# Kernel optimization log

Measured on AMD Instinct MI355X. Metric: run time of the kernel, lower is better.

The kernel has to match this reference:

```python
import jax, jax.numpy as jnp
import numpy as np

B, N, C = 4, 2048, 1024
H = 8
D = C // H  # head dim = 128
SCALE = D ** -0.5
EPS = 1e-5


def setup_inputs() -> dict:
    key = jax.random.key(0)
    ks = jax.random.split(key, 12)
    s = 0.02
    return {
        "x": jax.random.normal(ks[0], (B, N, C), jnp.float32),
        "ln1_g": jnp.ones((C,), jnp.float32),
        "ln1_b": jnp.zeros((C,), jnp.float32),
        "w_qkv": jax.random.normal(ks[1], (3 * C, C), jnp.float32) * s,  # torch Linear weight [out,in], no bias
        "w_proj": jax.random.normal(ks[2], (C, C), jnp.float32) * s,
        "b_proj": jnp.zeros((C,), jnp.float32),
        "ln2_g": jnp.ones((C,), jnp.float32),
        "ln2_b": jnp.zeros((C,), jnp.float32),
        "w1": jax.random.normal(ks[3], (C, C), jnp.float32) * s,
        "b1": jnp.full((C,), 0.1, jnp.float32),
        "w2": jax.random.normal(ks[4], (C, C), jnp.float32) * s,
        "b2": jnp.full((C,), 0.1, jnp.float32),
        "bn_g": jnp.ones((C,), jnp.float32),
        "bn_b": jnp.zeros((C,), jnp.float32),
        "bn_mean": jnp.zeros((C,), jnp.float32),
        "bn_var": jnp.ones((C,), jnp.float32),
    }


def _layernorm(x, g, b):
    mu = jnp.mean(x, axis=-1, keepdims=True)
    var = jnp.mean(jnp.square(x - mu), axis=-1, keepdims=True)
    return (x - mu) * jax.lax.rsqrt(var + EPS) * g + b


def reference(x, ln1_g, ln1_b, w_qkv, w_proj, b_proj, ln2_g, ln2_b,
              w1, b1, w2, b2, bn_g, bn_b, bn_mean, bn_var):
    # --- attention branch (pre-LN) ---
    h = _layernorm(x, ln1_g, ln1_b)
    qkv = h @ w_qkv.T                              # [B,N,3C]
    qkv = qkv.reshape(B, N, 3, H, D)
    q = qkv[:, :, 0].transpose(0, 2, 1, 3)         # [B,H,N,D]
    k = qkv[:, :, 1].transpose(0, 2, 1, 3)
    v = qkv[:, :, 2].transpose(0, 2, 1, 3)
    attn = jnp.einsum('bhnd,bhmd->bhnm', q, k) * SCALE
    attn = jax.nn.softmax(attn, axis=-1)
    o = jnp.einsum('bhnm,bhmd->bhnd', attn, v)     # [B,H,N,D]
    o = o.transpose(0, 2, 1, 3).reshape(B, N, C)
    x = x + (o @ w_proj.T + b_proj)

    # --- MLP branch (pre-LN), ELU + eval-mode BatchNorm ---
    h = _layernorm(x, ln2_g, ln2_b)
    h = jax.nn.elu(h @ w1.T + b1)
    h = jax.nn.elu(h @ w2.T + b2)
    h = (h - bn_mean) * jax.lax.rsqrt(bn_var + EPS) * bn_g + bn_b
    return x + h
```

## Files before the change

kernel.cpp:

```cpp
#include <hip/hip_runtime.h>
#include <hip/hip_bf16.h>

using u16 = unsigned short;
typedef __attribute__((ext_vector_type(8))) __bf16 bf16x8;
typedef __attribute__((ext_vector_type(4))) float f32x4;
typedef __attribute__((ext_vector_type(16))) float f32x16;
typedef __attribute__((ext_vector_type(4))) unsigned int u32x4;

#define LN_EPS 1e-5f
#define ATT_SCALE 0.08838834764831845f

__device__ __forceinline__ u16 f2bf(float f) {
    unsigned int u = __builtin_bit_cast(unsigned int, f);
    u += 0x7FFFu + ((u >> 16) & 1u);
    return (u16)(u >> 16);
}

__device__ __forceinline__ bf16x8 ld_frag(const u16* p) {
    return __builtin_bit_cast(bf16x8, *(const u32x4*)p);
}

__device__ __forceinline__ unsigned pack_bf2(float lo, float hi) {
    return __builtin_amdgcn_perm(__builtin_bit_cast(unsigned, hi),
                                 __builtin_bit_cast(unsigned, lo), 0x07060302u);
}

__device__ __forceinline__ void gl_lds(const u16* g, u16* l) {
    __builtin_amdgcn_global_load_lds((const __attribute__((address_space(1))) void*)g,
                                     (__attribute__((address_space(3))) void*)l, 16, 0, 0);
}

__global__ void cvt_all(const float* __restrict__ w_qkv, const float* __restrict__ w_proj,
                        const float* __restrict__ w1, const float* __restrict__ w2,
                        u16* __restrict__ out) {
    const int i = blockIdx.x * blockDim.x + threadIdx.x;
    const int n_qkv = 3072 * 1024 / 4, n_c = 1024 * 1024 / 4;
    const float* src;
    int j = i;
    if (j < n_qkv) { src = w_qkv; }
    else if ((j -= n_qkv) < n_c) { src = w_proj; }
    else if ((j -= n_c) < n_c)   { src = w1; }
    else { j -= n_c; src = w2; }
    const float4 v = ((const float4*)src)[j];
    ushort4 o;
    o.x = f2bf(v.x); o.y = f2bf(v.y); o.z = f2bf(v.z); o.w = f2bf(v.w);
    ((ushort4*)out)[i] = o;
}

__global__ __launch_bounds__(256)
void ln_kernel(const float* __restrict__ x, const float* __restrict__ g,
               const float* __restrict__ b, u16* __restrict__ out)
{
    const int row = blockIdx.x;
    const int t = threadIdx.x;
    const float4 v = ((const float4*)(x + (size_t)row * 1024))[t];
    float s  = v.x + v.y + v.z + v.w;
    float ss = v.x * v.x + v.y * v.y + v.z * v.z + v.w * v.w;
    #pragma unroll
    for (int d = 32; d > 0; d >>= 1) { s += __shfl_down(s, d); ss += __shfl_down(ss, d); }
    __shared__ float red[8];
    const int wave = t >> 6, lane = t & 63;
    if (lane == 0) { red[wave] = s; red[4 + wave] = ss; }
    __syncthreads();
    const float S  = red[0] + red[1] + red[2] + red[3];
    const float SS = red[4] + red[5] + red[6] + red[7];
    const float mu = S * (1.f / 1024.f);
    const float rstd = rsqrtf(SS * (1.f / 1024.f) - mu * mu + LN_EPS);
    const float4 gv = ((const float4*)g)[t];
    const float4 bv = ((const float4*)b)[t];
    ushort4 ov;
    ov.x = f2bf((v.x - mu) * rstd * gv.x + bv.x);
    ov.y = f2bf((v.y - mu) * rstd * gv.y + bv.y);
    ov.z = f2bf((v.z - mu) * rstd * gv.z + bv.z);
    ov.w = f2bf((v.w - mu) * rstd * gv.w + bv.w);
    ((ushort4*)(out + (size_t)row * 1024))[t] = ov;
}

__global__ __launch_bounds__(256, 3)
void gemm_qkv(const u16* __restrict__ A, const u16* __restrict__ Bw,
              u16* __restrict__ Cb, u16* __restrict__ Cv)
{
    const int K = 1024;
    __shared__ __align__(16) u16 As[128 * 32];
    __shared__ __align__(16) u16 Bs[128 * 32];

    const int tid  = threadIdx.x;
    const int wave = tid >> 6;
    const int lane = tid & 63;
    const int quad = lane >> 4;
    const int l16  = lane & 15;
    const int m0 = blockIdx.x * 128;
    const int n0 = blockIdx.y * 128;
    const int wm = (wave & 1) * 64;
    const int wn = (wave >> 1) * 64;

    f32x4 acc[4][4];
    #pragma unroll
    for (int i = 0; i < 4; i++)
        #pragma unroll
        for (int j = 0; j < 4; j++)
            acc[i][j] = f32x4{0.f, 0.f, 0.f, 0.f};

    const int srow = lane >> 2;
    const int scol = (lane & 3) * 8;
    const u16* gA0 = A  + (size_t)(m0 + wave * 32 + srow) * K + scol;
    const u16* gA1 = gA0 + (size_t)16 * K;
    const u16* gB0 = Bw + (size_t)(n0 + wave * 32 + srow) * K + scol;
    const u16* gB1 = gB0 + (size_t)16 * K;
    u16* lA0 = &As[(wave * 32) * 32];
    u16* lA1 = &As[(wave * 32 + 16) * 32];
    u16* lB0 = &Bs[(wave * 32) * 32];
    u16* lB1 = &Bs[(wave * 32 + 16) * 32];

    for (int k0 = 0; k0 < K; k0 += 32) {
        gl_lds(gA0 + k0, lA0);
        gl_lds(gA1 + k0, lA1);
        gl_lds(gB0 + k0, lB0);
        gl_lds(gB1 + k0, lB1);
        __syncthreads();
        bf16x8 af[4], bfv[4];
        #pragma unroll
        for (int i = 0; i < 4; i++) af[i]  = ld_frag(&As[(wm + i * 16 + l16) * 32 + quad * 8]);
        #pragma unroll
        for (int j = 0; j < 4; j++) bfv[j] = ld_frag(&Bs[(wn + j * 16 + l16) * 32 + quad * 8]);
        #pragma unroll
        for (int i = 0; i < 4; i++)
            #pragma unroll
            for (int j = 0; j < 4; j++)
                acc[i][j] = __builtin_amdgcn_mfma_f32_16x16x32_bf16(af[i], bfv[j], acc[i][j], 0, 0, 0);
        __syncthreads();
    }

    #pragma unroll
    for (int j = 0; j < 4; j++) {
        const int gn = n0 + wn + j * 16 + l16;
        if (gn < 2048) {
            const float qs = (gn < 1024) ? ATT_SCALE : 1.0f;
            #pragma unroll
            for (int i = 0; i < 4; i++) {
                const int gm0 = m0 + wm + i * 16 + quad * 4;
                #pragma unroll
                for (int r = 0; r < 4; r++)
                    Cb[(size_t)(gm0 + r) * 2048 + gn] = f2bf(acc[i][j][r] * qs);
            }
        } else {
            const int hh = (gn >> 7) & 7, dd = gn & 127;
            #pragma unroll
            for (int i = 0; i < 4; i++) {
                const int gm0 = m0 + wm + i * 16 + quad * 4;
                #pragma unroll
                for (int r = 0; r < 4; r++) {
                    const int tok = gm0 + r;
                    Cv[((size_t)((tok >> 11) * 8 + hh) * 128 + dd) * 2048 + (tok & 2047)] =
                        f2bf(acc[i][j][r]);
                }
            }
        }
    }
}

template <int EPI>
__global__ __launch_bounds__(256, 3)
void gemm_c(const u16* __restrict__ A, const u16* __restrict__ Bw,
            const float* __restrict__ bias, const float* __restrict__ res,
            float* __restrict__ Cf, u16* __restrict__ Cb,
            const float* __restrict__ bng, const float* __restrict__ bnb,
            const float* __restrict__ bnm, const float* __restrict__ bnv)
{
    const int N = 1024, K = 1024;
    __shared__ __align__(16) u16 As[128 * 32];
    __shared__ __align__(16) u16 Bs[128 * 32];

    const int tid  = threadIdx.x;
    const int wave = tid >> 6;
    const int lane = tid & 63;
    const int quad = lane >> 4;
    const int l16  = lane & 15;
    const int m0 = blockIdx.x * 128;
    const int n0 = blockIdx.y * 128;
    const int wm = (wave & 1) * 64;
    const int wn = (wave >> 1) * 64;

    f32x4 acc[4][4];
    #pragma unroll
    for (int i = 0; i < 4; i++)
        #pragma unroll
        for (int j = 0; j < 4; j++)
            acc[i][j] = f32x4{0.f, 0.f, 0.f, 0.f};

    const int srow = lane >> 2;
    const int scol = (lane & 3) * 8;
    const u16* gA0 = A  + (size_t)(m0 + wave * 32 + srow) * K + scol;
    const u16* gA1 = gA0 + (size_t)16 * K;
    const u16* gB0 = Bw + (size_t)(n0 + wave * 32 + srow) * K + scol;
    const u16* gB1 = gB0 + (size_t)16 * K;
    u16* lA0 = &As[(wave * 32) * 32];
    u16* lA1 = &As[(wave * 32 + 16) * 32];
    u16* lB0 = &Bs[(wave * 32) * 32];
    u16* lB1 = &Bs[(wave * 32 + 16) * 32];

    for (int k0 = 0; k0 < K; k0 += 32) {
        gl_lds(gA0 + k0, lA0);
        gl_lds(gA1 + k0, lA1);
        gl_lds(gB0 + k0, lB0);
        gl_lds(gB1 + k0, lB1);
        __syncthreads();
        bf16x8 af[4], bfv[4];
        #pragma unroll
        for (int i = 0; i < 4; i++) af[i]  = ld_frag(&As[(wm + i * 16 + l16) * 32 + quad * 8]);
        #pragma unroll
        for (int j = 0; j < 4; j++) bfv[j] = ld_frag(&Bs[(wn + j * 16 + l16) * 32 + quad * 8]);
        #pragma unroll
        for (int i = 0; i < 4; i++)
            #pragma unroll
            for (int j = 0; j < 4; j++)
                acc[i][j] = __builtin_amdgcn_mfma_f32_16x16x32_bf16(af[i], bfv[j], acc[i][j], 0, 0, 0);
        __syncthreads();
    }

    #pragma unroll
    for (int j = 0; j < 4; j++) {
        const int gn = n0 + wn + j * 16 + l16;
        float bs = bias[gn], sc = 0.f, sh = 0.f;
        if constexpr (EPI == 3) {
            const float iv = rsqrtf(bnv[gn] + LN_EPS);
            sc = bng[gn] * iv;
            sh = bnb[gn] - bnm[gn] * sc;
        }
        #pragma unroll
        for (int i = 0; i < 4; i++) {
            const int gm0 = m0 + wm + i * 16 + quad * 4;
            #pragma unroll
            for (int r = 0; r < 4; r++) {
                const size_t idx = (size_t)(gm0 + r) * N + gn;
                const float v = acc[i][j][r];
                if constexpr (EPI == 1) {
                    Cf[idx] = res[idx] + v + bs;
                } else if constexpr (EPI == 2) {
                    float t = v + bs;
                    t = t > 0.f ? t : (__expf(t) - 1.f);
                    Cb[idx] = f2bf(t);
                } else {
                    float t = v + bs;
                    t = t > 0.f ? t : (__expf(t) - 1.f);
                    t = t * sc + sh;
                    Cf[idx] = res[idx] + t;
                }
            }
        }
    }
}

__global__ __launch_bounds__(256, 2)
void attn_kernel(const u16* __restrict__ qk, const u16* __restrict__ vT, u16* __restrict__ o)
{
    __shared__ __align__(16) u16 smem[32768];

    const int tid  = threadIdx.x;
    const int wave = tid >> 6;
    const int lane = tid & 63;
    const int l32  = lane & 31;
    const int hl   = lane >> 5;
    const int id   = blockIdx.x;
    const int bh   = ((id >> 7) << 3) | (id & 7);
    const int qt   = (id >> 3) & 15;
    const int b    = bh >> 3, h = bh & 7;
    const size_t tok0 = (size_t)b * 2048;

    const u16* qptr = qk + h * 128;
    const u16* kptr = qk + 1024 + h * 128;
    const u16* vptr = vT + (size_t)bh * 128 * 2048;

    #pragma unroll
    for (int qq = 0; qq < 8; qq++) {
        const int s = qq * 256 + tid;
        const int r = s >> 4;
        const int cg = (s & 15) ^ (r & 7);
        const u16* g = qptr + (tok0 + qt * 128 + r) * 2048 + cg * 8;
        const int sb = 16384 + (qq * 256 + (tid & 192)) * 8;
        gl_lds(g, smem + sb);
    }
    __syncthreads();

    bf16x8 qf[8];
    {
        const int row = wave * 32 + l32;
        #pragma unroll
        for (int ks = 0; ks < 8; ks++) {
            const int c = (ks * 2 + hl) ^ (row & 7);
            qf[ks] = ld_frag(smem + 16384 + row * 128 + c * 8);
        }
    }

    f32x16 oacc[4];
    #pragma unroll
    for (int i = 0; i < 4; i++)
        #pragma unroll
        for (int e = 0; e < 16; e++) oacc[i][e] = 0.f;
    float l_acc = 0.f;

    {
        #pragma unroll
        for (int qq = 0; qq < 4; qq++) {
            const int s = qq * 256 + tid;
            const int rk = s >> 4, ck = (s & 15) ^ (rk & 7);
            gl_lds(kptr + (tok0 + rk) * 2048 + ck * 8,
                   smem + (qq * 256 + (tid & 192)) * 8);
            const int rv = s >> 3, cv = (s & 7) ^ (rv & 7);
            gl_lds(vptr + (size_t)rv * 2048 + cv * 8,
                   smem + 8192 + (qq * 256 + (tid & 192)) * 8);
        }
    }

    for (int kt = 0; kt < 32; kt++) {
        __syncthreads();

        if (kt + 1 < 32) {
            u16* nb = smem + ((kt + 1) & 1) * 16384;
            #pragma unroll
            for (int qq = 0; qq < 4; qq++) {
                const int s = qq * 256 + tid;
                const int rk = s >> 4, ck = (s & 15) ^ (rk & 7);
                gl_lds(kptr + (tok0 + (kt + 1) * 64 + rk) * 2048 + ck * 8,
                       nb + (qq * 256 + (tid & 192)) * 8);
                const int rv = s >> 3, cv = (s & 7) ^ (rv & 7);
                gl_lds(vptr + (size_t)rv * 2048 + (kt + 1) * 64 + cv * 8,
                       nb + 8192 + (qq * 256 + (tid & 192)) * 8);
            }
        }

        const u16* Ks = smem + (kt & 1) * 16384;
        const u16* Vs = Ks + 8192;

        f32x16 sacc[2];
        #pragma unroll
        for (int t = 0; t < 2; t++)
            #pragma unroll
            for (int e = 0; e < 16; e++) sacc[t][e] = 0.f;
        #pragma unroll
        for (int ks = 0; ks < 8; ks++) {
            #pragma unroll
            for (int mt = 0; mt < 2; mt++) {
                const int row = mt * 32 + l32;
                const int c = (ks * 2 + hl) ^ (row & 7);
                const bf16x8 kf = ld_frag(Ks + row * 128 + c * 8);
                sacc[mt] = __builtin_amdgcn_mfma_f32_32x32x16_bf16(kf, qf[ks], sacc[mt], 0, 0, 0);
            }
        }

        unsigned pk[2][8];
        #pragma unroll
        for (int t = 0; t < 2; t++) {
            #pragma unroll
            for (int r2 = 0; r2 < 8; r2++) {
                const float p0 = __expf(sacc[t][2 * r2]);
                const float p1 = __expf(sacc[t][2 * r2 + 1]);
                l_acc += p0 + p1;
                pk[t][r2] = pack_bf2(p0, p1);
            }
        }

        #pragma unroll
        for (int ks = 0; ks < 4; ks++) {
            const int t = ks >> 1;
            const int pb = (ks & 1) * 4;
            const unsigned s0 = (unsigned)__shfl_xor((int)pk[t][pb + 0], 32);
            const unsigned s1 = (unsigned)__shfl_xor((int)pk[t][pb + 1], 32);
            const unsigned s2 = (unsigned)__shfl_xor((int)pk[t][pb + 2], 32);
            const unsigned s3 = (unsigned)__shfl_xor((int)pk[t][pb + 3], 32);
            u32x4 pu;
            pu.x = hl ? s2 : pk[t][pb + 0];
            pu.y = hl ? s3 : pk[t][pb + 1];
            pu.z = hl ? pk[t][pb + 2] : s0;
            pu.w = hl ? pk[t][pb + 3] : s1;
            const bf16x8 pf = __builtin_bit_cast(bf16x8, pu);
            #pragma unroll
            for (int dt = 0; dt < 4; dt++) {
                const int row = dt * 32 + l32;
                const int c = (ks * 2 + hl) ^ (row & 7);
                const bf16x8 vf = ld_frag(Vs + row * 64 + c * 8);
                oacc[dt] = __builtin_amdgcn_mfma_f32_32x32x16_bf16(vf, pf, oacc[dt], 0, 0, 0);
            }
        }
    }

    __syncthreads();
    u16* Ot = smem;
    const float lt  = l_acc + __shfl_xor(l_acc, 32);
    const float inv = 1.0f / lt;
    const int qloc = wave * 32 + l32;
    #pragma unroll
    for (int dt = 0; dt < 4; dt++) {
        #pragma unroll
        for (int r2 = 0; r2 < 8; r2++) {
            const float v0 = oacc[dt][2 * r2] * inv;
            const float v1 = oacc[dt][2 * r2 + 1] * inv;
            const int dp = dt * 32 + 4 * hl + 2 * (r2 & 1) + 8 * (r2 >> 1);
            *(unsigned*)(Ot + qloc * 136 + dp) = pack_bf2(v0, v1);
        }
    }
    __syncthreads();
    const int qr = tid >> 1;
    const int hh = tid & 1;
    const u16* src = Ot + qr * 136 + hh * 64;
    u16* dst = o + (tok0 + qt * 128 + qr) * 1024 + h * 128 + hh * 64;
    #pragma unroll
    for (int c = 0; c < 8; c++)
        *(u32x4*)(dst + c * 8) = *(const u32x4*)(src + c * 8);
}

extern "C" void kernel_launch(void* const* d_in, const int* in_sizes, int n_in,
                              void* d_out, int out_size, void* d_ws, size_t ws_size,
                              hipStream_t stream)
{
    const float* x      = (const float*)d_in[0];
    const float* ln1_g  = (const float*)d_in[1];
    const float* ln1_b  = (const float*)d_in[2];
    const float* w_qkv  = (const float*)d_in[3];
    const float* w_proj = (const float*)d_in[4];
    const float* b_proj = (const float*)d_in[5];
    const float* ln2_g  = (const float*)d_in[6];
    const float* ln2_b  = (const float*)d_in[7];
    const float* w1     = (const float*)d_in[8];
    const float* b1     = (const float*)d_in[9];
    const float* w2     = (const float*)d_in[10];
    const float* b2     = (const float*)d_in[11];
    const float* bn_g   = (const float*)d_in[12];
    const float* bn_b   = (const float*)d_in[13];
    const float* bn_m   = (const float*)d_in[14];
    const float* bn_v   = (const float*)d_in[15];
    float* out = (float*)d_out;

    u16* wq   = (u16*)d_ws;
    u16* wp   = wq  + (size_t)3072 * 1024;
    u16* w1b  = wp  + (size_t)1024 * 1024;
    u16* w2b  = w1b + (size_t)1024 * 1024;
    u16* hbuf = w2b + (size_t)1024 * 1024;
    u16* qkb  = hbuf + (size_t)8192 * 1024;
    u16* vTb  = qkb + (size_t)8192 * 2048;
    u16* obuf = vTb + (size_t)8192 * 1024;
    float* x1 = (float*)(obuf + (size_t)8192 * 1024);

    cvt_all<<<6144, 256, 0, stream>>>(w_qkv, w_proj, w1, w2, wq);

    ln_kernel<<<8192, 256, 0, stream>>>(x, ln1_g, ln1_b, hbuf);

    gemm_qkv<<<dim3(64, 24), 256, 0, stream>>>(hbuf, wq, qkb, vTb);

    attn_kernel<<<512, 256, 0, stream>>>(qkb, vTb, obuf);

    gemm_c<1><<<dim3(64, 8), 256, 0, stream>>>(obuf, wp,
        b_proj, x, x1, nullptr, nullptr, nullptr, nullptr, nullptr);

    ln_kernel<<<8192, 256, 0, stream>>>(x1, ln2_g, ln2_b, hbuf);

    gemm_c<2><<<dim3(64, 8), 256, 0, stream>>>(hbuf, w1b,
        b1, nullptr, nullptr, obuf, nullptr, nullptr, nullptr, nullptr);

    gemm_c<3><<<dim3(64, 8), 256, 0, stream>>>(obuf, w2b,
        b2, x1, out, nullptr, bn_g, bn_b, bn_m, bn_v);
}
```

Measured before the change: 394.7 us.

## Split attention key tiles across two wave groups with LDS reduction

The attention block grows from 256 to 512 threads. Each of the two wave groups handles half of every 64-key tile, so each wave does one S MFMA chain instead of two. The partial O accumulators and row sums are then combined through LDS in two phases before normalisation and the bf16 store. It also swaps the shfl_xor lane exchange for permlane32_swap where that builtin exists. This is meant to raise occupancy and latency hiding, at the cost of extra barriers, a cross-group reduction, and a changed V swizzle.

```diff
diff --git a/kernel.cpp b/kernel.cpp
--- a/kernel.cpp
+++ b/kernel.cpp
@@ -6,6 +6,7 @@
 typedef __attribute__((ext_vector_type(4))) float f32x4;
 typedef __attribute__((ext_vector_type(16))) float f32x16;
 typedef __attribute__((ext_vector_type(4))) unsigned int u32x4;
+typedef __attribute__((ext_vector_type(2))) unsigned int uint2v;
 
 #define LN_EPS 1e-5f
 #define ATT_SCALE 0.08838834764831845f
@@ -251,13 +252,15 @@
     }
 }
 
-__global__ __launch_bounds__(256, 2)
+__global__ __launch_bounds__(512, 4)
 void attn_kernel(const u16* __restrict__ qk, const u16* __restrict__ vT, u16* __restrict__ o)
 {
     __shared__ __align__(16) u16 smem[32768];
 
     const int tid  = threadIdx.x;
     const int wave = tid >> 6;
+    const int g    = wave & 3;
+    const int kh   = wave >> 2;
     const int lane = tid & 63;
     const int l32  = lane & 31;
     const int hl   = lane >> 5;
@@ -272,25 +275,25 @@
     const u16* vptr = vT + (size_t)bh * 128 * 2048;
 
     #pragma unroll
-    for (int qq = 0; qq < 8; qq++) {
-        const int s = qq * 256 + tid;
+    for (int qq = 0; qq < 4; qq++) {
+        const int s = qq * 512 + tid;
         const int r = s >> 4;
         const int cg = (s & 15) ^ (r & 7);
-        const u16* g = qptr + (tok0 + qt * 128 + r) * 2048 + cg * 8;
-        const int sb = 16384 + (qq * 256 + (tid & 192)) * 8;
-        gl_lds(g, smem + sb);
+        gl_lds(qptr + (tok0 + qt * 128 + r) * 2048 + cg * 8,
+               smem + (qq * 512 + (tid & 448)) * 8);
     }
     __syncthreads();
 
     bf16x8 qf[8];
     {
-        const int row = wave * 32 + l32;
+        const int qrow = g * 32 + l32;
         #pragma unroll
         for (int ks = 0; ks < 8; ks++) {
-            const int c = (ks * 2 + hl) ^ (row & 7);
-            qf[ks] = ld_frag(smem + 16384 + row * 128 + c * 8);
-        }
-    }
+            const int c = (ks * 2 + hl) ^ (qrow & 7);
+            qf[ks] = ld_frag(smem + qrow * 128 + c * 8);
+        }
+    }
+    __syncthreads();
 
     f32x16 oacc[4];
     #pragma unroll
@@ -299,114 +302,140 @@
         for (int e = 0; e < 16; e++) oacc[i][e] = 0.f;
     float l_acc = 0.f;
 
-    {
-        #pragma unroll
-        for (int qq = 0; qq < 4; qq++) {
-            const int s = qq * 256 + tid;
+    auto stage = [&](int kt, int bufb) {
+        #pragma unroll
+        for (int qq = 0; qq < 2; qq++) {
+            const int s = qq * 512 + tid;
             const int rk = s >> 4, ck = (s & 15) ^ (rk & 7);
-            gl_lds(kptr + (tok0 + rk) * 2048 + ck * 8,
-                   smem + (qq * 256 + (tid & 192)) * 8);
-            const int rv = s >> 3, cv = (s & 7) ^ (rv & 7);
-            gl_lds(vptr + (size_t)rv * 2048 + cv * 8,
-                   smem + 8192 + (qq * 256 + (tid & 192)) * 8);
-        }
-    }
+            gl_lds(kptr + (tok0 + kt * 64 + rk) * 2048 + ck * 8,
+                   smem + bufb + (qq * 512 + (tid & 448)) * 8);
+        }
+        #pragma unroll
+        for (int qq = 0; qq < 2; qq++) {
+            const int s = qq * 512 + tid;
+            const int rv = s >> 3, cc = (s & 7) ^ (rv & 3);
+            gl_lds(vptr + (size_t)rv * 2048 + kt * 64 + cc * 8,
+                   smem + bufb + 8192 + (qq * 512 + (tid & 448)) * 8);
+        }
+    };
+
+    stage(0, 0);
+
+    const int krow = kh * 32 + l32;
 
     for (int kt = 0; kt < 32; kt++) {
         __syncthreads();
 
-        if (kt + 1 < 32) {
-            u16* nb = smem + ((kt + 1) & 1) * 16384;
-            #pragma unroll
-            for (int qq = 0; qq < 4; qq++) {
-                const int s = qq * 256 + tid;
-                const int rk = s >> 4, ck = (s & 15) ^ (rk & 7);
-                gl_lds(kptr + (tok0 + (kt + 1) * 64 + rk) * 2048 + ck * 8,
-                       nb + (qq * 256 + (tid & 192)) * 8);
-                const int rv = s >> 3, cv = (s & 7) ^ (rv & 7);
-                gl_lds(vptr + (size_t)rv * 2048 + (kt + 1) * 64 + cv * 8,
-                       nb + 8192 + (qq * 256 + (tid & 192)) * 8);
-            }
-        }
+        if (kt + 1 < 32) stage(kt + 1, ((kt + 1) & 1) * 16384);
 
         const u16* Ks = smem + (kt & 1) * 16384;
         const u16* Vs = Ks + 8192;
 
-        f32x16 sacc[2];
-        #pragma unroll
-        for (int t = 0; t < 2; t++)
-            #pragma unroll
-            for (int e = 0; e < 16; e++) sacc[t][e] = 0.f;
+        f32x16 sacc;
+        #pragma unroll
+        for (int e = 0; e < 16; e++) sacc[e] = 0.f;
         #pragma unroll
         for (int ks = 0; ks < 8; ks++) {
-            #pragma unroll
-            for (int mt = 0; mt < 2; mt++) {
-                const int row = mt * 32 + l32;
-                const int c = (ks * 2 + hl) ^ (row & 7);
-                const bf16x8 kf = ld_frag(Ks + row * 128 + c * 8);
-                sacc[mt] = __builtin_amdgcn_mfma_f32_32x32x16_bf16(kf, qf[ks], sacc[mt], 0, 0, 0);
-            }
-        }
-
-        unsigned pk[2][8];
-        #pragma unroll
-        for (int t = 0; t < 2; t++) {
-            #pragma unroll
-            for (int r2 = 0; r2 < 8; r2++) {
-                const float p0 = __expf(sacc[t][2 * r2]);
-                const float p1 = __expf(sacc[t][2 * r2 + 1]);
-                l_acc += p0 + p1;
-                pk[t][r2] = pack_bf2(p0, p1);
-            }
-        }
-
-        #pragma unroll
-        for (int ks = 0; ks < 4; ks++) {
-            const int t = ks >> 1;
-            const int pb = (ks & 1) * 4;
-            const unsigned s0 = (unsigned)__shfl_xor((int)pk[t][pb + 0], 32);
-            const unsigned s1 = (unsigned)__shfl_xor((int)pk[t][pb + 1], 32);
-            const unsigned s2 = (unsigned)__shfl_xor((int)pk[t][pb + 2], 32);
-            const unsigned s3 = (unsigned)__shfl_xor((int)pk[t][pb + 3], 32);
+            const int c = (ks * 2 + hl) ^ (krow & 7);
+            const bf16x8 kf = ld_frag(Ks + krow * 128 + c * 8);
+            sacc = __builtin_amdgcn_mfma_f32_32x32x16_bf16(kf, qf[ks], sacc, 0, 0, 0);
+        }
+
+        unsigned pk[8];
+        #pragma unroll
+        for (int r2 = 0; r2 < 8; r2++) {
+            const float p0 = __expf(sacc[2 * r2]);
+            const float p1 = __expf(sacc[2 * r2 + 1]);
+            l_acc += p0 + p1;
+            pk[r2] = pack_bf2(p0, p1);
+        }
+
+        #pragma unroll
+        for (int ks2 = 0; ks2 < 2; ks2++) {
+            const int pb = ks2 * 4;
             u32x4 pu;
-            pu.x = hl ? s2 : pk[t][pb + 0];
-            pu.y = hl ? s3 : pk[t][pb + 1];
-            pu.z = hl ? pk[t][pb + 2] : s0;
-            pu.w = hl ? pk[t][pb + 3] : s1;
+#if __has_builtin(__builtin_amdgcn_permlane32_swap)
+            const uint2v r0 = __builtin_amdgcn_permlane32_swap(pk[pb + 0], pk[pb + 2], false, false);
+            const uint2v r1 = __builtin_amdgcn_permlane32_swap(pk[pb + 1], pk[pb + 3], false, false);
+            pu.x = r0.x; pu.y = r1.x; pu.z = r0.y; pu.w = r1.y;
+#else
+            const unsigned s0 = (unsigned)__shfl_xor((int)pk[pb + 0], 32);
+            const unsigned s1 = (unsigned)__shfl_xor((int)pk[pb + 1], 32);
+            const unsigned s2 = (unsigned)__shfl_xor((int)pk[pb + 2], 32);
+            const unsigned s3 = (unsigned)__shfl_xor((int)pk[pb + 3], 32);
+            pu.x = hl ? s2 : pk[pb + 0];
+            pu.y = hl ? s3 : pk[pb + 1];
+            pu.z = hl ? pk[pb + 2] : s0;
+            pu.w = hl ? pk[pb + 3] : s1;
+#endif
             const bf16x8 pf = __builtin_bit_cast(bf16x8, pu);
             #pragma unroll
             for (int dt = 0; dt < 4; dt++) {
                 const int row = dt * 32 + l32;
-                const int c = (ks * 2 + hl) ^ (row & 7);
-                const bf16x8 vf = ld_frag(Vs + row * 64 + c * 8);
+                const int p = kh * 4 + ((ks2 * 2 + hl) ^ (row & 3));
+                const bf16x8 vf = ld_frag(Vs + row * 64 + p * 8);
                 oacc[dt] = __builtin_amdgcn_mfma_f32_32x32x16_bf16(vf, pf, oacc[dt], 0, 0, 0);
             }
         }
     }
 
     __syncthreads();
+    float* M = (float*)smem;
+    const int mbase = g * 2112 + lane;
+    #pragma unroll
+    for (int ph = 0; ph < 2; ph++) {
+        if (ph) __syncthreads();
+        if (kh == 1) {
+            #pragma unroll
+            for (int dtl = 0; dtl < 2; dtl++)
+                #pragma unroll
+                for (int e = 0; e < 16; e++)
+                    M[mbase + (dtl * 16 + e) * 64] = oacc[ph * 2 + dtl][e];
+            if (ph == 0) M[mbase + 32 * 64] = l_acc;
+        }
+        __syncthreads();
+        if (kh == 0) {
+            #pragma unroll
+            for (int dtl = 0; dtl < 2; dtl++)
+                #pragma unroll
+                for (int e = 0; e < 16; e++)
+                    oacc[ph * 2 + dtl][e] += M[mbase + (dtl * 16 + e) * 64];
+            if (ph == 0) l_acc += M[mbase + 32 * 64];
+        }
+    }
+    __syncthreads();
+
+    float inv = 0.f;
+    if (kh == 0) {
+        const float lt = l_acc + __shfl_xor(l_acc, 32);
+        inv = 1.0f / lt;
+    }
     u16* Ot = smem;
-    const float lt  = l_acc + __shfl_xor(l_acc, 32);
-    const float inv = 1.0f / lt;
-    const int qloc = wave * 32 + l32;
-    #pragma unroll
-    for (int dt = 0; dt < 4; dt++) {
-        #pragma unroll
-        for (int r2 = 0; r2 < 8; r2++) {
-            const float v0 = oacc[dt][2 * r2] * inv;
-            const float v1 = oacc[dt][2 * r2 + 1] * inv;
-            const int dp = dt * 32 + 4 * hl + 2 * (r2 & 1) + 8 * (r2 >> 1);
-            *(unsigned*)(Ot + qloc * 136 + dp) = pack_bf2(v0, v1);
-        }
-    }
-    __syncthreads();
-    const int qr = tid >> 1;
-    const int hh = tid & 1;
-    const u16* src = Ot + qr * 136 + hh * 64;
-    u16* dst = o + (tok0 + qt * 128 + qr) * 1024 + h * 128 + hh * 64;
-    #pragma unroll
-    for (int c = 0; c < 8; c++)
-        *(u32x4*)(dst + c * 8) = *(const u32x4*)(src + c * 8);
+    #pragma unroll
+    for (int p = 0; p < 2; p++) {
+        if (p) __syncthreads();
+        if (kh == 0) {
+            #pragma unroll
+            for (int dtl = 0; dtl < 2; dtl++) {
+                const int dt = p * 2 + dtl;
+                #pragma unroll
+                for (int r2 = 0; r2 < 8; r2++) {
+                    const float v0 = oacc[dt][2 * r2] * inv;
+                    const float v1 = oacc[dt][2 * r2 + 1] * inv;
+                    const int dp = dtl * 32 + 4 * hl + 2 * (r2 & 1) + 8 * (r2 >> 1);
+                    *(unsigned*)(Ot + (g * 32 + l32) * 72 + dp) = pack_bf2(v0, v1);
+                }
+            }
+        }
+        __syncthreads();
+        const int qr = tid >> 2;
+        const int qu = tid & 3;
+        const u16* src = Ot + qr * 72 + qu * 16;
+        u16* dst = o + (tok0 + qt * 128 + qr) * 1024 + h * 128 + p * 64 + qu * 16;
+        #pragma unroll
+        for (int cc = 0; cc < 2; cc++)
+            *(u32x4*)(dst + cc * 8) = *(const u32x4*)(src + cc * 8);
+    }
 }
 
 extern "C" void kernel_launch(void* const* d_in, const int* in_sizes, int n_in,
@@ -447,7 +476,7 @@
 
     gemm_qkv<<<dim3(64, 24), 256, 0, stream>>>(hbuf, wq, qkb, vTb);
 
-    attn_kernel<<<512, 256, 0, stream>>>(qkb, vTb, obuf);
+    attn_kernel<<<512, 512, 0, stream>>>(qkb, vTb, obuf);
 
     gemm_c<1><<<dim3(64, 8), 256, 0, stream>>>(obuf, wp,
         b_proj, x, x1, nullptr, nullptr, nullptr, nullptr, nullptr);
```

Result: slower. 433.1 us (+9.7%).
